# Optimization experiments

Hardware: AMD Instinct MI355X
Metric: run time of the kernel (lower is better)

Reference implementation:

```python
import jax, jax.numpy as jnp
import numpy as np

E = 1024
H = 16
CH = E // H

def setup_inputs() -> dict:
    key = jax.random.key(0)
    ks = jax.random.split(key, 9)
    s = E ** -0.5
    return {
        'x': jax.random.normal(ks[0], (4, 2048, E), dtype=jnp.float32),
        'Wq': jax.random.normal(ks[1], (E, E), dtype=jnp.float32) * s,
        'bq': jnp.zeros((E,), dtype=jnp.float32),
        'Wk': jax.random.normal(ks[2], (E, E), dtype=jnp.float32) * s,
        'bk': jnp.zeros((E,), dtype=jnp.float32),
        'Wv': jax.random.normal(ks[3], (E, E), dtype=jnp.float32) * s,
        'bv': jnp.zeros((E,), dtype=jnp.float32),
        'Wo': jax.random.normal(ks[4], (E, E), dtype=jnp.float32) * s,
        'bo': jnp.zeros((E,), dtype=jnp.float32),
    }

def _split_heads(t):
    # [..., n, H*ch] -> [..., H, n, ch]
    b, n, e = t.shape
    return t.reshape(b, n, H, CH).transpose(0, 2, 1, 3)

def reference(x, Wq, bq, Wk, bk, Wv, bv, Wo, bo):
    scale = CH ** -0.5
    q = _split_heads(x @ Wq.T + bq)  # [b,H,n,ch]
    k = _split_heads(x @ Wk.T + bk)
    v = _split_heads(x @ Wv.T + bv)
    att = jnp.einsum('bhqc,bhkc->bhqk', q, k) * scale
    att = jax.nn.softmax(att, axis=-1)
    out = jnp.einsum('bhqk,bhkc->bhqc', att, v)  # [b,H,n,ch]
    b, h, n, c = out.shape
    out = out.transpose(0, 2, 1, 3).reshape(b, n, h * c)
    return out @ Wo.T + bo
```

## Files before the change

### kernel.cpp

```cpp
#include <hip/hip_runtime.h>
#include <stdint.h>

#define EMB   1024
#define NHEAD 16
#define CHD   64
#define NB    4
#define SEQ   2048
#define NTOK  (NB * SEQ)
#define KDIM  1024

typedef __attribute__((ext_vector_type(8))) short  bf16x8;
typedef __attribute__((ext_vector_type(4))) short  short4v;
typedef __attribute__((ext_vector_type(4))) float  f32x4;
typedef __attribute__((ext_vector_type(4))) float  float4v;

__device__ __forceinline__ short f2bf(float f) {
    unsigned int u = __float_as_uint(f);
    u += 0x7fffu + ((u >> 16) & 1u);
    return (short)(u >> 16);
}

__device__ __forceinline__ void async16(const short* g, short* l) {
    __builtin_amdgcn_global_load_lds((__attribute__((address_space(1))) void const*)g,
                                     (__attribute__((address_space(3))) void*)l, 16, 0, 0);
}

__global__ __launch_bounds__(256) void cvt_all(const float* __restrict__ x,
                                               const float* __restrict__ Wq,
                                               const float* __restrict__ Wk,
                                               const float* __restrict__ Wv,
                                               const float* __restrict__ Wo,
                                               short* __restrict__ xb,
                                               short* __restrict__ Wqb,
                                               short* __restrict__ Wkb,
                                               short* __restrict__ Wvb,
                                               short* __restrict__ Wob) {
    int bid = blockIdx.x;
    const float* src;
    short* dst;
    int idx;
    if (bid < 8192) {
        src = x; dst = xb; idx = bid * 256 + threadIdx.x;
    } else {
        int w  = (bid - 8192) >> 10;
        int lb = (bid - 8192) & 1023;
        src = (w == 0) ? Wq : (w == 1) ? Wk : (w == 2) ? Wv : Wo;
        dst = (w == 0) ? Wqb : (w == 1) ? Wkb : (w == 2) ? Wvb : Wob;
        idx = lb * 256 + threadIdx.x;
    }
    float4v v = ((const float4v*)src)[idx];
    short4v s;
    s.x = f2bf(v.x); s.y = f2bf(v.y); s.z = f2bf(v.z); s.w = f2bf(v.w);
    ((short4v*)dst)[idx] = s;
}

__device__ __forceinline__ void gemm_core(const short* __restrict__ Atile,
                                          const short* __restrict__ Btile,
                                          short* As, short* Bs, f32x4 acc[4][4]) {
    const int tid  = threadIdx.x;
    const int wave = tid >> 6, lane = tid & 63;
    const int quad = lane >> 4, l16 = lane & 15;
    const int wm = (wave >> 1) * 64, wn = (wave & 1) * 64;
    const int srow = lane >> 2;
    const int scol = (lane & 3) * 8;

    for (int k0 = 0; k0 < KDIM; k0 += 32) {
        __syncthreads();
#pragma unroll
        for (int c = 0; c < 2; ++c) {
            int chunk = wave * 2 + c;
            int row = chunk * 16 + srow;
            async16(Atile + (size_t)row * KDIM + k0 + scol, As + chunk * 512);
            async16(Btile + (size_t)row * KDIM + k0 + scol, Bs + chunk * 512);
        }
        __syncthreads();
        bf16x8 af[4], bfr[4];
#pragma unroll
        for (int i = 0; i < 4; ++i)
            af[i] = *(const bf16x8*)&As[(wm + i * 16 + l16) * 32 + quad * 8];
#pragma unroll
        for (int j = 0; j < 4; ++j)
            bfr[j] = *(const bf16x8*)&Bs[(wn + j * 16 + l16) * 32 + quad * 8];
#pragma unroll
        for (int i = 0; i < 4; ++i)
#pragma unroll
            for (int j = 0; j < 4; ++j)
                acc[i][j] = __builtin_amdgcn_mfma_f32_16x16x32_bf16(af[i], bfr[j], acc[i][j], 0, 0, 0);
    }
}

#define QSCALE 0.1803368801111204f
__global__ __launch_bounds__(256) void qkv_gemm(const short* __restrict__ xb,
                                                const short* __restrict__ Wqb,
                                                const short* __restrict__ Wkb,
                                                const short* __restrict__ Wvb,
                                                const float* __restrict__ bq,
                                                const float* __restrict__ bk,
                                                const float* __restrict__ bv,
                                                short* __restrict__ Qb,
                                                short* __restrict__ Kb,
                                                short* __restrict__ Vtb) {
    __shared__ short As[128 * 32], Bs[128 * 32];
    const int bm = blockIdx.x, bn = blockIdx.y;
    const int which = bn >> 3;
    const int ew = (bn & 7) * 128;
    const short* W    = (which == 0) ? Wqb : (which == 1) ? Wkb : Wvb;
    const float* bias = (which == 0) ? bq  : (which == 1) ? bk  : bv;
    const float sc    = (which == 0) ? QSCALE : 1.0f;

    const short* Xt = xb + (size_t)bm * 128 * KDIM;
    const short* Wt = W + (size_t)ew * KDIM;
    const short* Ap = (which == 2) ? Wt : Xt;
    const short* Bp = (which == 2) ? Xt : Wt;

    f32x4 acc[4][4];
    const f32x4 z = {0.f, 0.f, 0.f, 0.f};
#pragma unroll
    for (int i = 0; i < 4; ++i)
#pragma unroll
        for (int j = 0; j < 4; ++j) acc[i][j] = z;

    gemm_core(Ap, Bp, As, Bs, acc);

    const int lane = threadIdx.x & 63, wave = threadIdx.x >> 6;
    const int quad = lane >> 4, l16 = lane & 15;
    const int wm = (wave >> 1) * 64, wn = (wave & 1) * 64;

    if (which == 2) {
#pragma unroll
        for (int i = 0; i < 4; ++i)
#pragma unroll
            for (int j = 0; j < 4; ++j)
#pragma unroll
                for (int r = 0; r < 4; ++r) {
                    int e = ew + wm + i * 16 + quad * 4 + r;
                    int token = bm * 128 + wn + j * 16 + l16;
                    int bb = token >> 11, nn = token & 2047;
                    int hh = e >> 6, cc = e & 63;
                    Vtb[(((size_t)bb * NHEAD + hh) * CHD + cc) * SEQ + nn] =
                        f2bf(acc[i][j][r] + bias[e]);
                }
    } else {
        short* dst = which ? Kb : Qb;
#pragma unroll
        for (int i = 0; i < 4; ++i)
#pragma unroll
            for (int j = 0; j < 4; ++j)
#pragma unroll
                for (int r = 0; r < 4; ++r) {
                    int token = bm * 128 + wm + i * 16 + quad * 4 + r;
                    int bb = token >> 11, nn = token & 2047;
                    int e = ew + wn + j * 16 + l16;
                    int hh = e >> 6, cc = e & 63;
                    dst[(((size_t)bb * NHEAD + hh) * SEQ + nn) * CHD + cc] =
                        f2bf((acc[i][j][r] + bias[e]) * sc);
                }
    }
}

__global__ __launch_bounds__(256, 4) void attn(const short* __restrict__ Qb,
                                               const short* __restrict__ Kb,
                                               const short* __restrict__ Vtb,
                                               short* __restrict__ AOb) {
    __shared__ short Ks[16 * 512];
    __shared__ short Vs[16 * 512];

    const int qt = blockIdx.x;
    const int bh = blockIdx.y;
    const int tid = threadIdx.x, wave = tid >> 6, lane = tid & 63;
    const int quad = lane >> 4, l16 = lane & 15;

    const short* Kg = Kb  + (size_t)bh * SEQ * CHD;
    const short* Vg = Vtb + (size_t)bh * CHD * SEQ;

    const short* Qg = Qb + ((size_t)bh * SEQ + qt * 64 + wave * 16 + l16) * CHD;
    bf16x8 qf0 = *(const bf16x8*)(Qg + quad * 8);
    bf16x8 qf1 = *(const bf16x8*)(Qg + 32 + quad * 8);

    const int kr = lane >> 3, ku = (lane & 7) ^ kr;
    const int vr = lane >> 4, vu = (lane & 15) ^ (vr << 2);

    int koff[4], voff[4];
#pragma unroll
    for (int cc = 0; cc < 4; ++cc) {
        int c = wave * 4 + cc;
        int l = c * 8 + kr;
        int j = l >> 4, m = l & 15;
        int kvg = ((j >> 1) << 5) + ((m >> 2) << 3) + ((j & 1) << 2) + (m & 3);
        koff[cc] = kvg * CHD + ku * 8;
        voff[cc] = (c * 4 + vr) * SEQ + vu * 8;
    }

    const int krow = l16 & 7;
    const int kbase = ((l16 >> 3) * 512) + krow * 64;
    const short* kp0 = Ks + kbase + ((quad ^ krow) << 3);
    const short* kp1 = Ks + kbase + (((4 + quad) ^ krow) << 3);
    const int vrow = l16 & 3;
    const short* vp = Vs + (l16 >> 2) * 512 + vrow * 128 + quad * 8;

    const f32x4 zf = {0.f, 0.f, 0.f, 0.f};
    const bf16x8 onesv = {16256, 16256, 16256, 16256, 16256, 16256, 16256, 16256};
    f32x4 O[4];
#pragma unroll
    for (int nb = 0; nb < 4; ++nb) O[nb] = zf;
    f32x4 lacc = zf;

    const short* Kgp = Kg;
    const short* Vgp = Vg;

    for (int kt = 0; kt < 16; ++kt) {
        __syncthreads();
#pragma unroll
        for (int cc = 0; cc < 4; ++cc) {
            int c = wave * 4 + cc;
            async16(Kgp + koff[cc], Ks + c * 512);
            async16(Vgp + voff[cc], Vs + c * 512);
        }
        Kgp += 128 * CHD;
        Vgp += 128;
        __syncthreads();

        f32x4 sacc[8];
#pragma unroll
        for (int j = 0; j < 8; ++j) {
            bf16x8 k0 = *(const bf16x8*)(kp0 + j * 1024);
            bf16x8 k1 = *(const bf16x8*)(kp1 + j * 1024);
            f32x4 t = __builtin_amdgcn_mfma_f32_16x16x32_bf16(k0, qf0, zf, 0, 0, 0);
            sacc[j] = __builtin_amdgcn_mfma_f32_16x16x32_bf16(k1, qf1, t, 0, 0, 0);
        }

#pragma unroll
        for (int kk = 0; kk < 4; ++kk) {
            int d[4];
#pragma unroll
            for (int t = 0; t < 2; ++t) {
                f32x4 s4 = sacc[2 * kk + t];
                unsigned u0 = __float_as_uint(__builtin_amdgcn_exp2f(s4.x));
                unsigned u1 = __float_as_uint(__builtin_amdgcn_exp2f(s4.y));
                unsigned u2 = __float_as_uint(__builtin_amdgcn_exp2f(s4.z));
                unsigned u3 = __float_as_uint(__builtin_amdgcn_exp2f(s4.w));
                d[2 * t]     = __builtin_amdgcn_perm(u1, u0, 0x07060302u);
                d[2 * t + 1] = __builtin_amdgcn_perm(u3, u2, 0x07060302u);
            }
            union { int i[4]; bf16x8 v; } pf;
            pf.i[0] = d[0]; pf.i[1] = d[1]; pf.i[2] = d[2]; pf.i[3] = d[3];
            lacc = __builtin_amdgcn_mfma_f32_16x16x32_bf16(pf.v, onesv, lacc, 0, 0, 0);
            const short* vpk = vp + ((kk ^ vrow) << 5);
#pragma unroll
            for (int nb = 0; nb < 4; ++nb) {
                bf16x8 vf = *(const bf16x8*)(vpk + nb * 2048);
                O[nb] = __builtin_amdgcn_mfma_f32_16x16x32_bf16(pf.v, vf, O[nb], 0, 0, 0);
            }
        }
    }

    float linv[4];
#pragma unroll
    for (int r = 0; r < 4; ++r) linv[r] = 1.0f / lacc[r];

    const int b = bh >> 4, h = bh & 15;
#pragma unroll
    for (int nb = 0; nb < 4; ++nb)
#pragma unroll
        for (int r = 0; r < 4; ++r) {
            int n = qt * 64 + wave * 16 + quad * 4 + r;
            int cc = nb * 16 + l16;
            AOb[((size_t)b * SEQ + n) * EMB + h * CHD + cc] = f2bf(O[nb][r] * linv[r]);
        }
}

__global__ __launch_bounds__(256) void out_gemm(const short* __restrict__ AOb,
                                                const short* __restrict__ Wob,
                                                const float* __restrict__ bo,
                                                float* __restrict__ out) {
    __shared__ short As[128 * 32], Bs[128 * 32];
    const int bm = blockIdx.x, bn = blockIdx.y;

    f32x4 acc[4][4];
    const f32x4 z = {0.f, 0.f, 0.f, 0.f};
#pragma unroll
    for (int i = 0; i < 4; ++i)
#pragma unroll
        for (int j = 0; j < 4; ++j) acc[i][j] = z;

    gemm_core(AOb + (size_t)bm * 128 * KDIM, Wob + (size_t)bn * 128 * KDIM, As, Bs, acc);

    const int lane = threadIdx.x & 63, wave = threadIdx.x >> 6;
    const int quad = lane >> 4, l16 = lane & 15;
    const int wm = (wave >> 1) * 64, wn = (wave & 1) * 64;
#pragma unroll
    for (int i = 0; i < 4; ++i)
#pragma unroll
        for (int j = 0; j < 4; ++j)
#pragma unroll
            for (int r = 0; r < 4; ++r) {
                int token = bm * 128 + wm + i * 16 + quad * 4 + r;
                int e = bn * 128 + wn + j * 16 + l16;
                out[(size_t)token * EMB + e] = acc[i][j][r] + bo[e];
            }
}

extern "C" void kernel_launch(void* const* d_in, const int* in_sizes, int n_in,
                              void* d_out, int out_size, void* d_ws, size_t ws_size,
                              hipStream_t stream) {
    const float* x  = (const float*)d_in[0];
    const float* Wq = (const float*)d_in[1];
    const float* bq = (const float*)d_in[2];
    const float* Wk = (const float*)d_in[3];
    const float* bk = (const float*)d_in[4];
    const float* Wv = (const float*)d_in[5];
    const float* bv = (const float*)d_in[6];
    const float* Wo = (const float*)d_in[7];
    const float* bo = (const float*)d_in[8];

    char* ws = (char*)d_ws;
    short* xb  = (short*)(ws + 0);
    short* Wqb = (short*)(ws + (size_t)16 * 1024 * 1024);
    short* Wkb = (short*)(ws + (size_t)18 * 1024 * 1024);
    short* Wvb = (short*)(ws + (size_t)20 * 1024 * 1024);
    short* Wob = (short*)(ws + (size_t)22 * 1024 * 1024);
    short* Qb  = (short*)(ws + (size_t)24 * 1024 * 1024);
    short* Kb  = (short*)(ws + (size_t)40 * 1024 * 1024);
    short* Vtb = (short*)(ws + (size_t)56 * 1024 * 1024);
    short* AOb = (short*)(ws + (size_t)72 * 1024 * 1024);

    cvt_all<<<dim3(8192 + 4096), dim3(256), 0, stream>>>(x, Wq, Wk, Wv, Wo,
                                                         xb, Wqb, Wkb, Wvb, Wob);
    qkv_gemm<<<dim3(64, 24), dim3(256), 0, stream>>>(xb, Wqb, Wkb, Wvb, bq, bk, bv, Qb, Kb, Vtb);
    attn<<<dim3(32, 64), dim3(256), 0, stream>>>(Qb, Kb, Vtb, AOb);
    out_gemm<<<dim3(64, 8), dim3(256), 0, stream>>>(AOb, Wob, bo, (float*)d_out);
}
```

Measured before the change: 287.5 us.

## Rewrite attention with 32x32 MFMA tiles, two query groups per wave

Attention now uses 32x32x16 bf16 MFMAs with each wave covering 64 queries as two 32-row groups. Blocks shrink to 2 waves handling 128 queries. The row-sum is accumulated in VALU from the truncated bf16 exp values instead of an extra ones-vector MFMA. The aim is more reuse of each K and V fragment loaded from LDS and fewer MFMA issues per FLOP. In exchange, register pressure and the LDS load share per thread go up, and the wave count per block drops.

Result: slower. 358.9 us (+24.8%).

```diff
diff --git a/kernel.cpp b/kernel.cpp
--- a/kernel.cpp
+++ b/kernel.cpp
@@ -9,10 +9,11 @@
 #define NTOK  (NB * SEQ)
 #define KDIM  1024
 
-typedef __attribute__((ext_vector_type(8))) short  bf16x8;
-typedef __attribute__((ext_vector_type(4))) short  short4v;
-typedef __attribute__((ext_vector_type(4))) float  f32x4;
-typedef __attribute__((ext_vector_type(4))) float  float4v;
+typedef __attribute__((ext_vector_type(8)))  short bf16x8;
+typedef __attribute__((ext_vector_type(4)))  short short4v;
+typedef __attribute__((ext_vector_type(4)))  float f32x4;
+typedef __attribute__((ext_vector_type(16))) float f32x16;
+typedef __attribute__((ext_vector_type(4)))  float float4v;
 
 __device__ __forceinline__ short f2bf(float f) {
     unsigned int u = __float_as_uint(f);
@@ -158,7 +159,7 @@
     }
 }
 
-__global__ __launch_bounds__(256, 4) void attn(const short* __restrict__ Qb,
+__global__ __launch_bounds__(128, 2) void attn(const short* __restrict__ Qb,
                                                const short* __restrict__ Kb,
                                                const short* __restrict__ Vtb,
                                                short* __restrict__ AOb) {
@@ -168,42 +169,45 @@
     const int qt = blockIdx.x;
     const int bh = blockIdx.y;
     const int tid = threadIdx.x, wave = tid >> 6, lane = tid & 63;
-    const int quad = lane >> 4, l16 = lane & 15;
+    const int l31 = lane & 31, h = lane >> 5;
 
     const short* Kg = Kb  + (size_t)bh * SEQ * CHD;
     const short* Vg = Vtb + (size_t)bh * CHD * SEQ;
 
-    const short* Qg = Qb + ((size_t)bh * SEQ + qt * 64 + wave * 16 + l16) * CHD;
-    bf16x8 qf0 = *(const bf16x8*)(Qg + quad * 8);
-    bf16x8 qf1 = *(const bf16x8*)(Qg + 32 + quad * 8);
-
-    const int kr = lane >> 3, ku = (lane & 7) ^ kr;
-    const int vr = lane >> 4, vu = (lane & 15) ^ (vr << 2);
-
-    int koff[4], voff[4];
-#pragma unroll
-    for (int cc = 0; cc < 4; ++cc) {
-        int c = wave * 4 + cc;
-        int l = c * 8 + kr;
-        int j = l >> 4, m = l & 15;
-        int kvg = ((j >> 1) << 5) + ((m >> 2) << 3) + ((j & 1) << 2) + (m & 3);
-        koff[cc] = kvg * CHD + ku * 8;
-        voff[cc] = (c * 4 + vr) * SEQ + vu * 8;
-    }
-
-    const int krow = l16 & 7;
-    const int kbase = ((l16 >> 3) * 512) + krow * 64;
-    const short* kp0 = Ks + kbase + ((quad ^ krow) << 3);
-    const short* kp1 = Ks + kbase + (((4 + quad) ^ krow) << 3);
-    const int vrow = l16 & 3;
-    const short* vp = Vs + (l16 >> 2) * 512 + vrow * 128 + quad * 8;
-
-    const f32x4 zf = {0.f, 0.f, 0.f, 0.f};
-    const bf16x8 onesv = {16256, 16256, 16256, 16256, 16256, 16256, 16256, 16256};
-    f32x4 O[4];
-#pragma unroll
-    for (int nb = 0; nb < 4; ++nb) O[nb] = zf;
-    f32x4 lacc = zf;
+    bf16x8 qf[2][4];
+#pragma unroll
+    for (int g = 0; g < 2; ++g)
+#pragma unroll
+        for (int c = 0; c < 4; ++c)
+            qf[g][c] = *(const bf16x8*)(Qb + ((size_t)bh * SEQ + qt * 128 + wave * 64 + g * 32 + l31) * CHD
+                                        + c * 16 + h * 8);
+
+    int koff[8], voff[8];
+#pragma unroll
+    for (int cc = 0; cc < 8; ++cc) {
+        int c = wave * 8 + cc;
+        int l = c * 8 + (lane >> 3);
+        int w = l & 31, r = w & 3, hh = (w >> 2) & 1, t = w >> 3, T = l >> 5;
+        int gkv = 32 * T + 16 * (t >> 1) + 8 * hh + 4 * (t & 1) + 2 * (r >> 1) + (r & 1);
+        koff[cc] = gkv * CHD + (((lane & 7) ^ (l & 7)) << 3);
+        int ch = c * 4 + (lane >> 4);
+        voff[cc] = ch * SEQ + (((lane & 15) ^ (ch & 15)) << 3);
+    }
+
+    int kra[4];
+#pragma unroll
+    for (int c = 0; c < 4; ++c)
+        kra[c] = l31 * 64 + ((((2 * c + h) ^ (l31 & 7))) << 3);
+    int vra[2];
+#pragma unroll
+    for (int s = 0; s < 2; ++s)
+        vra[s] = l31 * 128 + ((((2 * s + h) ^ (l31 & 15))) << 3);
+
+    const f32x16 z16 = {0.f,0.f,0.f,0.f,0.f,0.f,0.f,0.f,0.f,0.f,0.f,0.f,0.f,0.f,0.f,0.f};
+    f32x16 O[2][2];
+    O[0][0] = z16; O[0][1] = z16; O[1][0] = z16; O[1][1] = z16;
+    f32x4 ls[2];
+    ls[0] = (f32x4){0.f,0.f,0.f,0.f}; ls[1] = (f32x4){0.f,0.f,0.f,0.f};
 
     const short* Kgp = Kg;
     const short* Vgp = Vg;
@@ -211,8 +215,8 @@
     for (int kt = 0; kt < 16; ++kt) {
         __syncthreads();
 #pragma unroll
-        for (int cc = 0; cc < 4; ++cc) {
-            int c = wave * 4 + cc;
+        for (int cc = 0; cc < 8; ++cc) {
+            int c = wave * 8 + cc;
             async16(Kgp + koff[cc], Ks + c * 512);
             async16(Vgp + voff[cc], Vs + c * 512);
         }
@@ -220,52 +224,78 @@
         Vgp += 128;
         __syncthreads();
 
-        f32x4 sacc[8];
-#pragma unroll
-        for (int j = 0; j < 8; ++j) {
-            bf16x8 k0 = *(const bf16x8*)(kp0 + j * 1024);
-            bf16x8 k1 = *(const bf16x8*)(kp1 + j * 1024);
-            f32x4 t = __builtin_amdgcn_mfma_f32_16x16x32_bf16(k0, qf0, zf, 0, 0, 0);
-            sacc[j] = __builtin_amdgcn_mfma_f32_16x16x32_bf16(k1, qf1, t, 0, 0, 0);
+#pragma unroll
+        for (int T = 0; T < 4; ++T) {
+            f32x16 s0, s1;
+            {
+                bf16x8 kf = *(const bf16x8*)(Ks + kra[0] + T * 2048);
+                s0 = __builtin_amdgcn_mfma_f32_32x32x16_bf16(kf, qf[0][0], z16, 0, 0, 0);
+                s1 = __builtin_amdgcn_mfma_f32_32x32x16_bf16(kf, qf[1][0], z16, 0, 0, 0);
+            }
+#pragma unroll
+            for (int c = 1; c < 4; ++c) {
+                bf16x8 kf = *(const bf16x8*)(Ks + kra[c] + T * 2048);
+                s0 = __builtin_amdgcn_mfma_f32_32x32x16_bf16(kf, qf[0][c], s0, 0, 0, 0);
+                s1 = __builtin_amdgcn_mfma_f32_32x32x16_bf16(kf, qf[1][c], s1, 0, 0, 0);
+            }
+
+            bf16x8 pf[2][2];
+#pragma unroll
+            for (int g = 0; g < 2; ++g) {
+                const f32x16 sg = g ? s1 : s0;
+#pragma unroll
+                for (int sg2 = 0; sg2 < 2; ++sg2) {
+                    unsigned u[8];
+#pragma unroll
+                    for (int e = 0; e < 8; ++e)
+                        u[e] = __float_as_uint(__builtin_amdgcn_exp2f(sg[sg2 * 8 + e]));
+                    union { int i[4]; bf16x8 v; } pk;
+                    pk.i[0] = __builtin_amdgcn_perm(u[1], u[0], 0x07060302u);
+                    pk.i[1] = __builtin_amdgcn_perm(u[3], u[2], 0x07060302u);
+                    pk.i[2] = __builtin_amdgcn_perm(u[5], u[4], 0x07060302u);
+                    pk.i[3] = __builtin_amdgcn_perm(u[7], u[6], 0x07060302u);
+                    pf[g][sg2] = pk.v;
+                    ls[g][0] += __uint_as_float(u[0] & 0xffff0000u) + __uint_as_float(u[4] & 0xffff0000u);
+                    ls[g][1] += __uint_as_float(u[1] & 0xffff0000u) + __uint_as_float(u[5] & 0xffff0000u);
+                    ls[g][2] += __uint_as_float(u[2] & 0xffff0000u) + __uint_as_float(u[6] & 0xffff0000u);
+                    ls[g][3] += __uint_as_float(u[3] & 0xffff0000u) + __uint_as_float(u[7] & 0xffff0000u);
+                }
+            }
+
+#pragma unroll
+            for (int sg2 = 0; sg2 < 2; ++sg2) {
+                int vo = (vra[sg2] ^ (T << 5));
+#pragma unroll
+                for (int ct = 0; ct < 2; ++ct) {
+                    bf16x8 vf = *(const bf16x8*)(Vs + vo + ct * 4096);
+                    O[0][ct] = __builtin_amdgcn_mfma_f32_32x32x16_bf16(pf[0][sg2], vf, O[0][ct], 0, 0, 0);
+                    O[1][ct] = __builtin_amdgcn_mfma_f32_32x32x16_bf16(pf[1][sg2], vf, O[1][ct], 0, 0, 0);
+                }
+            }
         }
-
-#pragma unroll
-        for (int kk = 0; kk < 4; ++kk) {
-            int d[4];
-#pragma unroll
-            for (int t = 0; t < 2; ++t) {
-                f32x4 s4 = sacc[2 * kk + t];
-                unsigned u0 = __float_as_uint(__builtin_amdgcn_exp2f(s4.x));
-                unsigned u1 = __float_as_uint(__builtin_amdgcn_exp2f(s4.y));
-                unsigned u2 = __float_as_uint(__builtin_amdgcn_exp2f(s4.z));
-                unsigned u3 = __float_as_uint(__builtin_amdgcn_exp2f(s4.w));
-                d[2 * t]     = __builtin_amdgcn_perm(u1, u0, 0x07060302u);
-                d[2 * t + 1] = __builtin_amdgcn_perm(u3, u2, 0x07060302u);
-            }
-            union { int i[4]; bf16x8 v; } pf;
-            pf.i[0] = d[0]; pf.i[1] = d[1]; pf.i[2] = d[2]; pf.i[3] = d[3];
-            lacc = __builtin_amdgcn_mfma_f32_16x16x32_bf16(pf.v, onesv, lacc, 0, 0, 0);
-            const short* vpk = vp + ((kk ^ vrow) << 5);
-#pragma unroll
-            for (int nb = 0; nb < 4; ++nb) {
-                bf16x8 vf = *(const bf16x8*)(vpk + nb * 2048);
-                O[nb] = __builtin_amdgcn_mfma_f32_16x16x32_bf16(pf.v, vf, O[nb], 0, 0, 0);
-            }
-        }
-    }
-
-    float linv[4];
-#pragma unroll
-    for (int r = 0; r < 4; ++r) linv[r] = 1.0f / lacc[r];
-
-    const int b = bh >> 4, h = bh & 15;
-#pragma unroll
-    for (int nb = 0; nb < 4; ++nb)
-#pragma unroll
-        for (int r = 0; r < 4; ++r) {
-            int n = qt * 64 + wave * 16 + quad * 4 + r;
-            int cc = nb * 16 + l16;
-            AOb[((size_t)b * SEQ + n) * EMB + h * CHD + cc] = f2bf(O[nb][r] * linv[r]);
+    }
+
+    float lt[2];
+#pragma unroll
+    for (int g = 0; g < 2; ++g) {
+        lt[g] = ls[g][0] + ls[g][1] + ls[g][2] + ls[g][3];
+        lt[g] += __shfl_xor(lt[g], 32);
+        lt[g] = 1.0f / lt[g];
+    }
+
+    const int b = bh >> 4, hd = bh & 15;
+#pragma unroll
+    for (int g = 0; g < 2; ++g)
+#pragma unroll
+        for (int reg = 0; reg < 16; ++reg) {
+            int qr = (reg & 3) + 8 * (reg >> 2) + 4 * h;
+            float li = __shfl(lt[g], qr);
+            int n = qt * 128 + wave * 64 + g * 32 + qr;
+#pragma unroll
+            for (int ct = 0; ct < 2; ++ct) {
+                int ccol = ct * 32 + l31;
+                AOb[((size_t)b * SEQ + n) * EMB + hd * CHD + ccol] = f2bf(O[g][ct][reg] * li);
+            }
         }
 }
 
@@ -327,6 +357,6 @@
     cvt_all<<<dim3(8192 + 4096), dim3(256), 0, stream>>>(x, Wq, Wk, Wv, Wo,
                                                          xb, Wqb, Wkb, Wvb, Wob);
     qkv_gemm<<<dim3(64, 24), dim3(256), 0, stream>>>(xb, Wqb, Wkb, Wvb, bq, bk, bv, Qb, Kb, Vtb);
-    attn<<<dim3(32, 64), dim3(256), 0, stream>>>(Qb, Kb, Vtb, AOb);
+    attn<<<dim3(16, 64), dim3(128), 0, stream>>>(Qb, Kb, Vtb, AOb);
     out_gemm<<<dim3(64, 8), dim3(256), 0, stream>>>(AOb, Wob, bo, (float*)d_out);
 }
```
